# Optimization experiments

Hardware: AMD Instinct MI355X
Metric: run time of the kernel (lower is better)

Reference implementation:

```python
import jax, jax.numpy as jnp
import numpy as np

# Daubechies-4 (db2) orthonormal filters (Dwork-style wtDaubechies2 coefficients)
_S3 = np.sqrt(3.0)
_DEN = 4.0 * np.sqrt(2.0)
_LO = np.array([1.0 + _S3, 3.0 + _S3, 3.0 - _S3, 1.0 - _S3], dtype=np.float32) / _DEN
_HI = np.array([1.0 - _S3, _S3 - 3.0, 3.0 + _S3, -(1.0 + _S3)], dtype=np.float32) / _DEN


def _up2(a, axis):
    """Upsample by 2 along `axis` (zeros at odd positions)."""
    a = jnp.moveaxis(a, axis, -1)
    u = jnp.stack([a, jnp.zeros_like(a)], axis=-1).reshape(*a.shape[:-1], 2 * a.shape[-1])
    return jnp.moveaxis(u, -1, axis)


def _cconv(u, f, axis):
    """Circular convolution y[n] = sum_k f[k] u[n-k] (filter length 4)."""
    return sum(float(f[k]) * jnp.roll(u, k, axis=axis) for k in range(len(f)))


def _ilevel(wt):
    """One level of separable 2D inverse db2 (periodized, orthonormal -> W^T)."""
    H, W = wt.shape
    # invert along rows (axis 0): low half on top, high half on bottom
    t = _cconv(_up2(wt[: H // 2], 0), _LO, 0) + _cconv(_up2(wt[H // 2 :], 0), _HI, 0)
    # invert along cols (axis 1)
    return _cconv(_up2(t[:, : W // 2], 1), _LO, 1) + _cconv(_up2(t[:, W // 2 :], 1), _HI, 1)


def _iwt2(wt, levels):
    if levels > 1:
        H, W = wt.shape
        sub = _iwt2(wt[: H // 2, : W // 2], levels - 1)
        wt = wt.at[: H // 2, : W // 2].set(sub)
    return _ilevel(wt)


def setup_inputs() -> dict:
    key = jax.random.key(0)
    k1, k2, k3 = jax.random.split(key, 3)
    N = 4096
    x = jax.random.normal(k1, (1, N, N), dtype=jnp.float32)
    mask = jax.random.uniform(k2, (N, N), dtype=jnp.float32)
    b = jax.random.normal(k3, (N, N), dtype=jnp.float32)
    wavSplit = jnp.ones((4, 4), dtype=jnp.int32)  # 4x4 split -> 3 levels
    return {"x": x, "mask": mask, "b": b, "wavSplit": wavSplit}


def reference(x, mask, b, wavSplit):
    # levels derived from the (static) split shape: 2^(L-1) == split side
    levels = int(np.log2(wavSplit.shape[0])) + 1
    return _iwt2(jnp.squeeze(x), levels)
```

## Files before the change

kernel.cpp:

```cpp
#include <hip/hip_runtime.h>

#define H_0 0.48296291314469025f
#define H_1 0.8365163037378079f
#define H_2 0.22414386804201336f
#define H_3 (-0.12940952255092145f)
#define G_0 (-0.12940952255092145f)
#define G_1 (-0.22414386804201336f)
#define G_2 0.8365163037378079f
#define G_3 (-0.48296291314469025f)


__device__ __forceinline__ float4 rowpass4(float h0, float h2, float g0, float g2,
                                           const float4& P, const float4& Q,
                                           const float4& R, const float4& T) {
    return make_float4(h0 * P.x + h2 * Q.x + g0 * R.x + g2 * T.x,
                       h0 * P.y + h2 * Q.y + g0 * R.y + g2 * T.y,
                       h0 * P.z + h2 * Q.z + g0 * R.z + g2 * T.z,
                       h0 * P.w + h2 * Q.w + g0 * R.w + g2 * T.w);
}

__device__ __forceinline__ void colpass_store(float* __restrict__ dst,
                                              const float4 L, const float Lm1,
                                              const float4 Hi, const float Hm1) {
    float4 s0, s1;
    s0.x = H_0 * L.x + H_2 * Lm1 + G_0 * Hi.x + G_2 * Hm1;
    s0.y = H_1 * L.x + H_3 * Lm1 + G_1 * Hi.x + G_3 * Hm1;
    s0.z = H_0 * L.y + H_2 * L.x + G_0 * Hi.y + G_2 * Hi.x;
    s0.w = H_1 * L.y + H_3 * L.x + G_1 * Hi.y + G_3 * Hi.x;
    s1.x = H_0 * L.z + H_2 * L.y + G_0 * Hi.z + G_2 * Hi.y;
    s1.y = H_1 * L.z + H_3 * L.y + G_1 * Hi.z + G_3 * Hi.y;
    s1.z = H_0 * L.w + H_2 * L.z + G_0 * Hi.w + G_2 * Hi.z;
    s1.w = H_1 * L.w + H_3 * L.z + G_1 * Hi.w + G_3 * Hi.z;
    *reinterpret_cast<float4*>(dst) = s0;
    *reinterpret_cast<float4*>(dst + 4) = s1;
}

__global__ __launch_bounds__(256) void iwt_fused_roll(
    const float* __restrict__ x, int ldx,
    const float* __restrict__ sub, int ldsub,
    float* __restrict__ out, int ldo,
    int S2, int segShift, int K) {
    const int lane = threadIdx.x & 63;
    const int wid = (blockIdx.x * 256 + threadIdx.x) >> 6;
    const int seg = wid & ((1 << segShift) - 1);
    const int m0 = (wid >> segShift) * K;
    const int cl = (seg << 8) + (lane << 2);
    int lw = (seg << 8) - 1;
    if (lw < 0) lw = S2 - 1;

    const bool hasSub = (sub != nullptr);
    const float* __restrict__ pA = hasSub ? sub : x;
    const int ldA = hasSub ? ldsub : ldx;

    const int mp0 = (m0 == 0) ? (S2 - 1) : (m0 - 1);
    float4 Ap = *reinterpret_cast<const float4*>(pA + (size_t)mp0 * ldA + cl);
    float4 Bp = *reinterpret_cast<const float4*>(x + (size_t)(S2 + mp0) * ldx + cl);
    float4 Cp = *reinterpret_cast<const float4*>(x + (size_t)mp0 * ldx + S2 + cl);
    float4 Dp = *reinterpret_cast<const float4*>(x + (size_t)(S2 + mp0) * ldx + S2 + cl);
    float ap = pA[(size_t)mp0 * ldA + lw];
    float bp = x[(size_t)(S2 + mp0) * ldx + lw];
    float cp = x[(size_t)mp0 * ldx + S2 + lw];
    float dp = x[(size_t)(S2 + mp0) * ldx + S2 + lw];

    for (int i = 0; i < K; ++i) {
        const int m = m0 + i;
        const float4 A = *reinterpret_cast<const float4*>(pA + (size_t)m * ldA + cl);
        const float4 B = *reinterpret_cast<const float4*>(x + (size_t)(S2 + m) * ldx + cl);
        const float4 C = *reinterpret_cast<const float4*>(x + (size_t)m * ldx + S2 + cl);
        const float4 D = *reinterpret_cast<const float4*>(x + (size_t)(S2 + m) * ldx + S2 + cl);
        const float a = pA[(size_t)m * ldA + lw];
        const float b = x[(size_t)(S2 + m) * ldx + lw];
        const float c = x[(size_t)m * ldx + S2 + lw];
        const float d = x[(size_t)(S2 + m) * ldx + S2 + lw];

        const float4 TL0 = rowpass4(H_0, H_2, G_0, G_2, A, Ap, B, Bp);
        const float4 TL1 = rowpass4(H_1, H_3, G_1, G_3, A, Ap, B, Bp);
        const float4 TH0 = rowpass4(H_0, H_2, G_0, G_2, C, Cp, D, Dp);
        const float4 TH1 = rowpass4(H_1, H_3, G_1, G_3, C, Cp, D, Dp);

        const float tl0 = H_0 * a + H_2 * ap + G_0 * b + G_2 * bp;
        const float tl1 = H_1 * a + H_3 * ap + G_1 * b + G_3 * bp;
        const float th0 = H_0 * c + H_2 * cp + G_0 * d + G_2 * dp;
        const float th1 = H_1 * c + H_3 * cp + G_1 * d + G_3 * dp;

        float pL0 = __shfl_up(TL0.w, 1); if (lane == 0) pL0 = tl0;
        float pL1 = __shfl_up(TL1.w, 1); if (lane == 0) pL1 = tl1;
        float pH0 = __shfl_up(TH0.w, 1); if (lane == 0) pH0 = th0;
        float pH1 = __shfl_up(TH1.w, 1); if (lane == 0) pH1 = th1;

        float* o0 = out + (size_t)(2 * m) * ldo + 2 * cl;
        colpass_store(o0, TL0, pL0, TH0, pH0);
        colpass_store(o0 + ldo, TL1, pL1, TH1, pH1);

        Ap = A; Bp = B; Cp = C; Dp = D;
        ap = a; bp = b; cp = c; dp = d;
    }
}

extern "C" void kernel_launch(void* const* d_in, const int* in_sizes, int n_in,
                              void* d_out, int out_size, void* d_ws, size_t ws_size,
                              hipStream_t stream) {
    const float* x = (const float*)d_in[0];
    float* out = (float*)d_out;
    float* buf1 = (float*)d_ws;
    float* buf2 = (float*)((char*)d_ws + ((size_t)16 << 20));

    const int N = 4096;

    iwt_fused_roll<<<256, 256, 0, stream>>>(x, N, nullptr, 0, buf1, 1024, 512, 1, 1);
    iwt_fused_roll<<<512, 256, 0, stream>>>(x, N, buf1, 1024, buf2, 2048, 1024, 2, 2);
    iwt_fused_roll<<<512, 256, 0, stream>>>(x, N, buf2, 2048, out, N, 2048, 3, 8);
}
```

Baseline: 43.64 us.

## Template row count, replace lane shuffle with per-lane neighbor loads, double grid

```diff
diff --git a/kernel.cpp b/kernel.cpp
--- a/kernel.cpp
+++ b/kernel.cpp
@@ -35,18 +35,18 @@
     *reinterpret_cast<float4*>(dst + 4) = s1;
 }
 
-__global__ __launch_bounds__(256) void iwt_fused_roll(
+template <int K>
+__global__ __launch_bounds__(256) void iwt_roll(
     const float* __restrict__ x, int ldx,
     const float* __restrict__ sub, int ldsub,
     float* __restrict__ out, int ldo,
-    int S2, int segShift, int K) {
+    int S2, int segShift) {
     const int lane = threadIdx.x & 63;
     const int wid = (blockIdx.x * 256 + threadIdx.x) >> 6;
     const int seg = wid & ((1 << segShift) - 1);
     const int m0 = (wid >> segShift) * K;
     const int cl = (seg << 8) + (lane << 2);
-    int lw = (seg << 8) - 1;
-    if (lw < 0) lw = S2 - 1;
+    const int cm1 = (cl == 0) ? (S2 - 1) : (cl - 1);
 
     const bool hasSub = (sub != nullptr);
     const float* __restrict__ pA = hasSub ? sub : x;
@@ -57,40 +57,36 @@
     float4 Bp = *reinterpret_cast<const float4*>(x + (size_t)(S2 + mp0) * ldx + cl);
     float4 Cp = *reinterpret_cast<const float4*>(x + (size_t)mp0 * ldx + S2 + cl);
     float4 Dp = *reinterpret_cast<const float4*>(x + (size_t)(S2 + mp0) * ldx + S2 + cl);
-    float ap = pA[(size_t)mp0 * ldA + lw];
-    float bp = x[(size_t)(S2 + mp0) * ldx + lw];
-    float cp = x[(size_t)mp0 * ldx + S2 + lw];
-    float dp = x[(size_t)(S2 + mp0) * ldx + S2 + lw];
+    float ap = pA[(size_t)mp0 * ldA + cm1];
+    float bp = x[(size_t)(S2 + mp0) * ldx + cm1];
+    float cp = x[(size_t)mp0 * ldx + S2 + cm1];
+    float dp = x[(size_t)(S2 + mp0) * ldx + S2 + cm1];
 
+#pragma unroll
     for (int i = 0; i < K; ++i) {
         const int m = m0 + i;
         const float4 A = *reinterpret_cast<const float4*>(pA + (size_t)m * ldA + cl);
         const float4 B = *reinterpret_cast<const float4*>(x + (size_t)(S2 + m) * ldx + cl);
         const float4 C = *reinterpret_cast<const float4*>(x + (size_t)m * ldx + S2 + cl);
         const float4 D = *reinterpret_cast<const float4*>(x + (size_t)(S2 + m) * ldx + S2 + cl);
-        const float a = pA[(size_t)m * ldA + lw];
-        const float b = x[(size_t)(S2 + m) * ldx + lw];
-        const float c = x[(size_t)m * ldx + S2 + lw];
-        const float d = x[(size_t)(S2 + m) * ldx + S2 + lw];
+        const float a = pA[(size_t)m * ldA + cm1];
+        const float b = x[(size_t)(S2 + m) * ldx + cm1];
+        const float c = x[(size_t)m * ldx + S2 + cm1];
+        const float d = x[(size_t)(S2 + m) * ldx + S2 + cm1];
 
         const float4 TL0 = rowpass4(H_0, H_2, G_0, G_2, A, Ap, B, Bp);
         const float4 TL1 = rowpass4(H_1, H_3, G_1, G_3, A, Ap, B, Bp);
         const float4 TH0 = rowpass4(H_0, H_2, G_0, G_2, C, Cp, D, Dp);
         const float4 TH1 = rowpass4(H_1, H_3, G_1, G_3, C, Cp, D, Dp);
 
-        const float tl0 = H_0 * a + H_2 * ap + G_0 * b + G_2 * bp;
-        const float tl1 = H_1 * a + H_3 * ap + G_1 * b + G_3 * bp;
-        const float th0 = H_0 * c + H_2 * cp + G_0 * d + G_2 * dp;
-        const float th1 = H_1 * c + H_3 * cp + G_1 * d + G_3 * dp;
-
-        float pL0 = __shfl_up(TL0.w, 1); if (lane == 0) pL0 = tl0;
-        float pL1 = __shfl_up(TL1.w, 1); if (lane == 0) pL1 = tl1;
-        float pH0 = __shfl_up(TH0.w, 1); if (lane == 0) pH0 = th0;
-        float pH1 = __shfl_up(TH1.w, 1); if (lane == 0) pH1 = th1;
+        const float mL0 = H_0 * a + H_2 * ap + G_0 * b + G_2 * bp;
+        const float mL1 = H_1 * a + H_3 * ap + G_1 * b + G_3 * bp;
+        const float mH0 = H_0 * c + H_2 * cp + G_0 * d + G_2 * dp;
+        const float mH1 = H_1 * c + H_3 * cp + G_1 * d + G_3 * dp;
 
         float* o0 = out + (size_t)(2 * m) * ldo + 2 * cl;
-        colpass_store(o0, TL0, pL0, TH0, pH0);
-        colpass_store(o0 + ldo, TL1, pL1, TH1, pH1);
+        colpass_store(o0, TL0, mL0, TH0, mH0);
+        colpass_store(o0 + ldo, TL1, mL1, TH1, mH1);
 
         Ap = A; Bp = B; Cp = C; Dp = D;
         ap = a; bp = b; cp = c; dp = d;
@@ -107,7 +103,7 @@
 
     const int N = 4096;
 
-    iwt_fused_roll<<<256, 256, 0, stream>>>(x, N, nullptr, 0, buf1, 1024, 512, 1, 1);
-    iwt_fused_roll<<<512, 256, 0, stream>>>(x, N, buf1, 1024, buf2, 2048, 1024, 2, 2);
-    iwt_fused_roll<<<512, 256, 0, stream>>>(x, N, buf2, 2048, out, N, 2048, 3, 8);
+    iwt_roll<1><<<256, 256, 0, stream>>>(x, N, nullptr, 0, buf1, 1024, 512, 1);
+    iwt_roll<1><<<1024, 256, 0, stream>>>(x, N, buf1, 1024, buf2, 2048, 1024, 2);
+    iwt_roll<4><<<1024, 256, 0, stream>>>(x, N, buf2, 2048, out, N, 2048, 3);
 }
```

After: 45.32 us. 1.04x slower.
